# Kernel tuning notes

Measured on AMD Instinct MI355X. Metric: run time of the kernel, lower is better.

The kernel has to match this reference:

```python
import jax, jax.numpy as jnp
import numpy as np

N_NODES = 100000
N_EDGES = 3200000
IN_F, HID_F, OUT_F = 128, 64, 32
NEG_SLOPE = 0.2


def setup_inputs() -> dict:
    key = jax.random.key(0)
    ks = jax.random.split(key, 10)
    glorot = lambda k, shape: jax.random.normal(k, shape, jnp.float32) * jnp.sqrt(2.0 / (shape[0] + shape[-1]))
    x = jax.random.normal(ks[0], (N_NODES, IN_F), jnp.float32)
    edge_index = jax.random.randint(ks[1], (2, N_EDGES), 0, N_NODES, jnp.int64)
    return {
        "x": x,
        "edge_index": edge_index,
        "W1": glorot(ks[2], (IN_F, HID_F)),
        "att_src1": glorot(ks[3], (HID_F,)),
        "att_dst1": glorot(ks[4], (HID_F,)),
        "b1": jnp.zeros((HID_F,), jnp.float32),
        "W2": glorot(ks[5], (HID_F, OUT_F)),
        "att_src2": glorot(ks[6], (OUT_F,)),
        "att_dst2": glorot(ks[7], (OUT_F,)),
        "b2": jnp.zeros((OUT_F,), jnp.float32),
    }


def _segment_softmax(logits, seg, num_segments):
    m = jax.ops.segment_max(logits, seg, num_segments=num_segments)
    e = jnp.exp(logits - m[seg])
    s = jax.ops.segment_sum(e, seg, num_segments=num_segments)
    return e / s[seg]


def _gat_conv(x, src, dst, W, a_src, a_dst, b, n):
    h = x @ W                                    # [N, F]
    logits = jax.nn.leaky_relu((h @ a_src)[src] + (h @ a_dst)[dst], NEG_SLOPE)  # [E]
    att = _segment_softmax(logits, dst, n)       # softmax over incoming edges per dst
    out = jax.ops.segment_sum(h[src] * att[:, None], dst, num_segments=n)
    return out + b


def reference(x, edge_index, W1, att_src1, att_dst1, b1, W2, att_src2, att_dst2, b2):
    n = x.shape[0]
    loops = jnp.arange(n, dtype=edge_index.dtype)
    src = jnp.concatenate([edge_index[0], loops])  # PyG GATConv adds self-loops
    dst = jnp.concatenate([edge_index[1], loops])
    h = _gat_conv(x, src, dst, W1, att_src1, att_dst1, b1, n)
    h = jax.nn.relu(h)
    h = _gat_conv(h, src, dst, W2, att_src2, att_dst2, b2, n)
    return jax.nn.softmax(h, axis=1)
```

## Files before the change

### kernel.cpp

```cpp
#include <hip/hip_runtime.h>

#define N_NODES 100000
#define N_EDGES 3200000
#define ET (N_EDGES + N_NODES)
#define IN_F 128
#define HID_F 64
#define OUT_F 32
#define NEG_SLOPE 0.2f

#define NB 391
#define CHUNK_A 8192
#define BLOCKS_A ((ET + CHUNK_A - 1) / CHUNK_A)
#define BKT_CAP 12288


__global__ __launch_bounds__(256) void histB_kernel(const int* __restrict__ ei,
                                                    int* __restrict__ bcnt) {
    __shared__ int lh[NB];
    for (int i = threadIdx.x; i < NB; i += 256) lh[i] = 0;
    __syncthreads();
    int stride = gridDim.x * 256;
    for (int e = blockIdx.x * 256 + threadIdx.x; e < N_EDGES; e += stride) {
        int dst = ei[N_EDGES + e];
        atomicAdd(&lh[dst >> 8], 1);
    }
    __syncthreads();
    for (int i = threadIdx.x; i < NB; i += 256) {
        int c = lh[i];
        if (c) atomicAdd(&bcnt[i], c);
    }
}


__global__ __launch_bounds__(512) void scanB_kernel(const int* __restrict__ bcnt,
                                                    int* __restrict__ bucket_base,
                                                    int* __restrict__ gcursor,
                                                    int* __restrict__ row_ptr) {
    __shared__ int a[NB];
    int t = threadIdx.x;
    int selfc = 0, cnt = 0;
    if (t < NB) {
        selfc = min(256, N_NODES - (t << 8));
        cnt = bcnt[t] + selfc;
        a[t] = cnt;
    }
    __syncthreads();
    for (int off = 1; off < NB; off <<= 1) {
        int v = 0;
        if (t < NB && t >= off) v = a[t - off];
        __syncthreads();
        if (t < NB) a[t] += v;
        __syncthreads();
    }
    if (t < NB) {
        int base = a[t] - cnt;
        bucket_base[t] = base;
        gcursor[t] = base;
    }
    if (t == 0) { bucket_base[NB] = ET; row_ptr[N_NODES] = ET; }
}


__global__ __launch_bounds__(256) void partA_kernel(const int* __restrict__ ei,
                                                    int* __restrict__ gcursor,
                                                    unsigned* __restrict__ staging) {
    __shared__ int cnt[NB];
    __shared__ int inc[NB];
    __shared__ int delta[NB];
    __shared__ unsigned stg[CHUNK_A];
    __shared__ unsigned short bkt[CHUNK_A];
    int t = threadIdx.x;
    int begin = blockIdx.x * CHUNK_A;
    int n = min(CHUNK_A, ET - begin);

    for (int i = t; i < NB; i += 256) cnt[i] = 0;
    __syncthreads();

    for (int i = t; i < n; i += 256) {
        int e = begin + i;
        int dst = (e < N_EDGES) ? ei[N_EDGES + e] : (e - N_EDGES);
        atomicAdd(&cnt[dst >> 8], 1);
    }
    __syncthreads();

    for (int i = t; i < NB; i += 256) inc[i] = cnt[i];
    __syncthreads();
    for (int off = 1; off < NB; off <<= 1) {
        int i0 = t, i1 = t + 256;
        int v0 = (i0 < NB && i0 >= off) ? inc[i0 - off] : 0;
        int v1 = (i1 < NB && i1 >= off) ? inc[i1 - off] : 0;
        __syncthreads();
        if (i0 < NB) inc[i0] += v0;
        if (i1 < NB) inc[i1] += v1;
        __syncthreads();
    }

    for (int i = t; i < NB; i += 256) {
        int c = cnt[i];
        int ls = inc[i] - c;
        int g = (c > 0) ? atomicAdd(&gcursor[i], c) : 0;
        delta[i] = g - ls;
        cnt[i] = ls;
    }
    __syncthreads();

    for (int i = t; i < n; i += 256) {
        int e = begin + i;
        int src, dst;
        if (e < N_EDGES) { src = ei[e]; dst = ei[N_EDGES + e]; }
        else             { src = dst = e - N_EDGES; }
        int b = dst >> 8;
        int pos = atomicAdd(&cnt[b], 1);
        stg[pos] = ((unsigned)(dst & 255) << 17) | (unsigned)src;
        bkt[pos] = (unsigned short)b;
    }
    __syncthreads();

    for (int i = t; i < n; i += 256) {
        staging[delta[bkt[i]] + i] = stg[i];
    }
}


__global__ __launch_bounds__(256) void partB_kernel(const unsigned* __restrict__ staging,
                                                    const int* __restrict__ bucket_base,
                                                    int* __restrict__ row_ptr,
                                                    int* __restrict__ src_sorted) {
    __shared__ int out_s[BKT_CAP];
    __shared__ int a[256];
    __shared__ int cur[256];
    int b = blockIdx.x, t = threadIdx.x;
    int nb0 = b << 8;
    int nn = min(256, N_NODES - nb0);
    int g0 = bucket_base[b];
    int g1 = bucket_base[b + 1];
    int n = g1 - g0;

    cur[t] = 0;
    __syncthreads();
    for (int i = t; i < n; i += 256)
        atomicAdd(&cur[staging[g0 + i] >> 17], 1);
    __syncthreads();

    int v = cur[t];
    a[t] = v;
    __syncthreads();
    for (int off = 1; off < 256; off <<= 1) {
        int w = (t >= off) ? a[t - off] : 0;
        __syncthreads();
        a[t] += w;
        __syncthreads();
    }
    int pref = a[t] - v;
    cur[t] = pref;
    if (t < nn) row_ptr[nb0 + t] = g0 + pref;
    __syncthreads();

    for (int i = t; i < n; i += 256) {
        unsigned u = staging[g0 + i];
        int pos = atomicAdd(&cur[u >> 17], 1);
        out_s[pos] = (int)(u & 0x1FFFFu);
    }
    __syncthreads();
    for (int i = t; i < n; i += 256)
        src_sorted[g0 + i] = out_s[i];
}


__global__ __launch_bounds__(256) void gemm1_kernel(const float* __restrict__ x,
                                                    const float* __restrict__ W,
                                                    const float* __restrict__ a_src,
                                                    const float* __restrict__ a_dst,
                                                    float* __restrict__ h,
                                                    float* __restrict__ as,
                                                    float* __restrict__ ad) {
    __shared__ float Wl[IN_F * HID_F];
    __shared__ float Xl[64 * 132];
    int t = threadIdx.x;
    int base = blockIdx.x * 64;

    for (int i = t; i < IN_F * HID_F / 4; i += 256)
        ((float4*)Wl)[i] = ((const float4*)W)[i];
#pragma unroll
    for (int i = 0; i < 8; ++i) {
        int f4 = t + 256 * i;
        int r = f4 >> 5, c4 = f4 & 31;
        int gr = base + r; if (gr >= N_NODES) gr = N_NODES - 1;
        ((float4*)Xl)[r * 33 + c4] = ((const float4*)(x + (size_t)gr * IN_F))[c4];
    }
    __syncthreads();

    int tx = t & 15, ty = t >> 4;
    int col = tx * 4, row0 = ty * 4;

    float4 acc0 = {0,0,0,0}, acc1 = {0,0,0,0}, acc2 = {0,0,0,0}, acc3 = {0,0,0,0};

#pragma unroll 4
    for (int k = 0; k < IN_F; k += 4) {
        float4 xv0 = *(const float4*)&Xl[(row0 + 0) * 132 + k];
        float4 xv1 = *(const float4*)&Xl[(row0 + 1) * 132 + k];
        float4 xv2 = *(const float4*)&Xl[(row0 + 2) * 132 + k];
        float4 xv3 = *(const float4*)&Xl[(row0 + 3) * 132 + k];
        float4 wv0 = *(const float4*)&Wl[(k + 0) * HID_F + col];
        float4 wv1 = *(const float4*)&Wl[(k + 1) * HID_F + col];
        float4 wv2 = *(const float4*)&Wl[(k + 2) * HID_F + col];
        float4 wv3 = *(const float4*)&Wl[(k + 3) * HID_F + col];
#define G1STEP(A, XV) \
        A.x = fmaf(XV.x, wv0.x, A.x); A.y = fmaf(XV.x, wv0.y, A.y); \
        A.z = fmaf(XV.x, wv0.z, A.z); A.w = fmaf(XV.x, wv0.w, A.w); \
        A.x = fmaf(XV.y, wv1.x, A.x); A.y = fmaf(XV.y, wv1.y, A.y); \
        A.z = fmaf(XV.y, wv1.z, A.z); A.w = fmaf(XV.y, wv1.w, A.w); \
        A.x = fmaf(XV.z, wv2.x, A.x); A.y = fmaf(XV.z, wv2.y, A.y); \
        A.z = fmaf(XV.z, wv2.z, A.z); A.w = fmaf(XV.z, wv2.w, A.w); \
        A.x = fmaf(XV.w, wv3.x, A.x); A.y = fmaf(XV.w, wv3.y, A.y); \
        A.z = fmaf(XV.w, wv3.z, A.z); A.w = fmaf(XV.w, wv3.w, A.w);
        G1STEP(acc0, xv0) G1STEP(acc1, xv1) G1STEP(acc2, xv2) G1STEP(acc3, xv3)
#undef G1STEP
    }

    float4 av = *(const float4*)&a_src[col];
    float4 dv = *(const float4*)&a_dst[col];
#define G1OUT(I, A) { \
        int grow = base + row0 + I; \
        float vs = A.x*av.x + A.y*av.y + A.z*av.z + A.w*av.w; \
        float vd = A.x*dv.x + A.y*dv.y + A.z*dv.z + A.w*dv.w; \
        vs += __shfl_xor(vs, 1, 64); vd += __shfl_xor(vd, 1, 64); \
        vs += __shfl_xor(vs, 2, 64); vd += __shfl_xor(vd, 2, 64); \
        vs += __shfl_xor(vs, 4, 64); vd += __shfl_xor(vd, 4, 64); \
        vs += __shfl_xor(vs, 8, 64); vd += __shfl_xor(vd, 8, 64); \
        if (grow < N_NODES) { \
            *(float4*)&h[(size_t)grow * HID_F + col] = A; \
            if (tx == 0) { as[grow] = vs; ad[grow] = vd; } \
        } }
    G1OUT(0, acc0) G1OUT(1, acc1) G1OUT(2, acc2) G1OUT(3, acc3)
#undef G1OUT
}


__global__ __launch_bounds__(256) void agg1_kernel(const float* __restrict__ h,
                                                   const float* __restrict__ as,
                                                   const float* __restrict__ ad,
                                                   const int* __restrict__ row_ptr,
                                                   const int* __restrict__ src_sorted,
                                                   const float* __restrict__ b,
                                                   float* __restrict__ r1) {
    int n = blockIdx.x * 4 + (threadIdx.x >> 6);
    int lane = threadIdx.x & 63;
    if (n >= N_NODES) return;
    int beg = row_ptr[n], end = row_ptr[n + 1];
    int deg = end - beg;
    float adn = ad[n];

    int e0 = beg + lane;
    int sidx = 0;
    float l = -1e30f;
    if (e0 < end) {
        sidx = src_sorted[e0];
        float t = as[sidx] + adn;
        l = (t >= 0.f) ? t : NEG_SLOPE * t;
    }
    float m = l;
    float s = (e0 < end) ? 1.f : 0.f;
    for (int e = beg + lane + 64; e < end; e += 64) {
        int s2 = src_sorted[e];
        float t = as[s2] + adn;
        t = (t >= 0.f) ? t : NEG_SLOPE * t;
        float mN = fmaxf(m, t);
        s = s * __expf(m - mN) + __expf(t - mN);
        m = mN;
    }
    for (int off = 32; off > 0; off >>= 1) {
        float mo = __shfl_xor(m, off, 64);
        float so = __shfl_xor(s, off, 64);
        float mN = fmaxf(m, mo);
        s = s * __expf(m - mN) + so * __expf(mo - mN);
        m = mN;
    }
    float inv = 1.f / s;
    float w = __expf(l - m) * inv;

    int g  = lane >> 4;
    int fo = (lane & 15) * 4;
    float4 acc = {0.f, 0.f, 0.f, 0.f};
    int rounds = (min(deg, 64) + 3) >> 2;
    int R4 = (rounds + 3) & ~3;
    for (int k = 0; k < R4; k += 4) {
        float w0 = __shfl(w, (k + 0) * 4 + g, 64);
        float w1 = __shfl(w, (k + 1) * 4 + g, 64);
        float w2 = __shfl(w, (k + 2) * 4 + g, 64);
        float w3 = __shfl(w, (k + 3) * 4 + g, 64);
        int   s0 = __shfl(sidx, (k + 0) * 4 + g, 64);
        int   s1 = __shfl(sidx, (k + 1) * 4 + g, 64);
        int   s2 = __shfl(sidx, (k + 2) * 4 + g, 64);
        int   s3 = __shfl(sidx, (k + 3) * 4 + g, 64);
        float4 p0 = *(const float4*)&h[s0 * HID_F + fo];
        float4 p1 = *(const float4*)&h[s1 * HID_F + fo];
        float4 p2 = *(const float4*)&h[s2 * HID_F + fo];
        float4 p3 = *(const float4*)&h[s3 * HID_F + fo];
        acc.x = fmaf(p0.x, w0, acc.x); acc.y = fmaf(p0.y, w0, acc.y);
        acc.z = fmaf(p0.z, w0, acc.z); acc.w = fmaf(p0.w, w0, acc.w);
        acc.x = fmaf(p1.x, w1, acc.x); acc.y = fmaf(p1.y, w1, acc.y);
        acc.z = fmaf(p1.z, w1, acc.z); acc.w = fmaf(p1.w, w1, acc.w);
        acc.x = fmaf(p2.x, w2, acc.x); acc.y = fmaf(p2.y, w2, acc.y);
        acc.z = fmaf(p2.z, w2, acc.z); acc.w = fmaf(p2.w, w2, acc.w);
        acc.x = fmaf(p3.x, w3, acc.x); acc.y = fmaf(p3.y, w3, acc.y);
        acc.z = fmaf(p3.z, w3, acc.z); acc.w = fmaf(p3.w, w3, acc.w);
    }
    for (int cb = beg + 64; cb < end; cb += 64) {
        int e = cb + lane;
        float wr = 0.f;
        int sr = 0;
        if (e < end) {
            sr = src_sorted[e];
            float t = as[sr] + adn;
            t = (t >= 0.f) ? t : NEG_SLOPE * t;
            wr = __expf(t - m) * inv;
        }
        int cnt = min(64, end - cb);
        int rr = (cnt + 3) >> 2;
        for (int k = 0; k < rr; ++k) {
            int sl = k * 4 + g;
            float wk = __shfl(wr, sl, 64);
            int   sk = __shfl(sr, sl, 64);
            float4 hv = *(const float4*)&h[sk * HID_F + fo];
            acc.x = fmaf(hv.x, wk, acc.x);
            acc.y = fmaf(hv.y, wk, acc.y);
            acc.z = fmaf(hv.z, wk, acc.z);
            acc.w = fmaf(hv.w, wk, acc.w);
        }
    }
    acc.x += __shfl_xor(acc.x, 16, 64); acc.x += __shfl_xor(acc.x, 32, 64);
    acc.y += __shfl_xor(acc.y, 16, 64); acc.y += __shfl_xor(acc.y, 32, 64);
    acc.z += __shfl_xor(acc.z, 16, 64); acc.z += __shfl_xor(acc.z, 32, 64);
    acc.w += __shfl_xor(acc.w, 16, 64); acc.w += __shfl_xor(acc.w, 32, 64);

    if (lane < 16) {
        float4 bv = *(const float4*)&b[fo];
        float4 v;
        v.x = fmaxf(acc.x + bv.x, 0.f);
        v.y = fmaxf(acc.y + bv.y, 0.f);
        v.z = fmaxf(acc.z + bv.z, 0.f);
        v.w = fmaxf(acc.w + bv.w, 0.f);
        *(float4*)&r1[n * HID_F + fo] = v;
    }
}


__global__ __launch_bounds__(256) void gemm2_kernel(const float* __restrict__ r1,
                                                    const float* __restrict__ W,
                                                    const float* __restrict__ a_src,
                                                    const float* __restrict__ a_dst,
                                                    float* __restrict__ h2,
                                                    float* __restrict__ as2,
                                                    float* __restrict__ ad2) {
    __shared__ float Wl[HID_F * OUT_F];
    __shared__ float Xl[128 * 68];
    int t = threadIdx.x;
    int base = blockIdx.x * 128;

    for (int i = t; i < HID_F * OUT_F / 4; i += 256)
        ((float4*)Wl)[i] = ((const float4*)W)[i];
#pragma unroll
    for (int i = 0; i < 8; ++i) {
        int f4 = t + 256 * i;
        int r = f4 >> 4, c4 = f4 & 15;
        int gr = base + r; if (gr >= N_NODES) gr = N_NODES - 1;
        ((float4*)Xl)[r * 17 + c4] = ((const float4*)(r1 + (size_t)gr * HID_F))[c4];
    }
    __syncthreads();

    int tx = t & 7, ty = t >> 3;
    int col = tx * 4, row0 = ty * 4;

    float4 acc0 = {0,0,0,0}, acc1 = {0,0,0,0}, acc2 = {0,0,0,0}, acc3 = {0,0,0,0};

#pragma unroll 4
    for (int k = 0; k < HID_F; k += 4) {
        float4 xv0 = *(const float4*)&Xl[(row0 + 0) * 68 + k];
        float4 xv1 = *(const float4*)&Xl[(row0 + 1) * 68 + k];
        float4 xv2 = *(const float4*)&Xl[(row0 + 2) * 68 + k];
        float4 xv3 = *(const float4*)&Xl[(row0 + 3) * 68 + k];
        float4 wv0 = *(const float4*)&Wl[(k + 0) * OUT_F + col];
        float4 wv1 = *(const float4*)&Wl[(k + 1) * OUT_F + col];
        float4 wv2 = *(const float4*)&Wl[(k + 2) * OUT_F + col];
        float4 wv3 = *(const float4*)&Wl[(k + 3) * OUT_F + col];
#define G2STEP(A, XV) \
        A.x = fmaf(XV.x, wv0.x, A.x); A.y = fmaf(XV.x, wv0.y, A.y); \
        A.z = fmaf(XV.x, wv0.z, A.z); A.w = fmaf(XV.x, wv0.w, A.w); \
        A.x = fmaf(XV.y, wv1.x, A.x); A.y = fmaf(XV.y, wv1.y, A.y); \
        A.z = fmaf(XV.y, wv1.z, A.z); A.w = fmaf(XV.y, wv1.w, A.w); \
        A.x = fmaf(XV.z, wv2.x, A.x); A.y = fmaf(XV.z, wv2.y, A.y); \
        A.z = fmaf(XV.z, wv2.z, A.z); A.w = fmaf(XV.z, wv2.w, A.w); \
        A.x = fmaf(XV.w, wv3.x, A.x); A.y = fmaf(XV.w, wv3.y, A.y); \
        A.z = fmaf(XV.w, wv3.z, A.z); A.w = fmaf(XV.w, wv3.w, A.w);
        G2STEP(acc0, xv0) G2STEP(acc1, xv1) G2STEP(acc2, xv2) G2STEP(acc3, xv3)
#undef G2STEP
    }

    float4 av = *(const float4*)&a_src[col];
    float4 dv = *(const float4*)&a_dst[col];
#define G2OUT(I, A) { \
        int grow = base + row0 + I; \
        float vs = A.x*av.x + A.y*av.y + A.z*av.z + A.w*av.w; \
        float vd = A.x*dv.x + A.y*dv.y + A.z*dv.z + A.w*dv.w; \
        vs += __shfl_xor(vs, 1, 64); vd += __shfl_xor(vd, 1, 64); \
        vs += __shfl_xor(vs, 2, 64); vd += __shfl_xor(vd, 2, 64); \
        vs += __shfl_xor(vs, 4, 64); vd += __shfl_xor(vd, 4, 64); \
        if (grow < N_NODES) { \
            *(float4*)&h2[(size_t)grow * OUT_F + col] = A; \
            if (tx == 0) { as2[grow] = vs; ad2[grow] = vd; } \
        } }
    G2OUT(0, acc0) G2OUT(1, acc1) G2OUT(2, acc2) G2OUT(3, acc3)
#undef G2OUT
}


__global__ __launch_bounds__(256) void agg2_kernel(const float* __restrict__ h2,
                                                   const float* __restrict__ as2,
                                                   const float* __restrict__ ad2,
                                                   const int* __restrict__ row_ptr,
                                                   const int* __restrict__ src_sorted,
                                                   const float* __restrict__ b2,
                                                   float* __restrict__ out) {
    int n = blockIdx.x * 4 + (threadIdx.x >> 6);
    int lane = threadIdx.x & 63;
    if (n >= N_NODES) return;
    int beg = row_ptr[n], end = row_ptr[n + 1];
    int deg = end - beg;
    float adn = ad2[n];

    int e0 = beg + lane;
    int sidx = 0;
    float l = -1e30f;
    if (e0 < end) {
        sidx = src_sorted[e0];
        float t = as2[sidx] + adn;
        l = (t >= 0.f) ? t : NEG_SLOPE * t;
    }
    float m = l;
    float s = (e0 < end) ? 1.f : 0.f;
    for (int e = beg + lane + 64; e < end; e += 64) {
        int s2 = src_sorted[e];
        float t = as2[s2] + adn;
        t = (t >= 0.f) ? t : NEG_SLOPE * t;
        float mN = fmaxf(m, t);
        s = s * __expf(m - mN) + __expf(t - mN);
        m = mN;
    }
    for (int off = 32; off > 0; off >>= 1) {
        float mo = __shfl_xor(m, off, 64);
        float so = __shfl_xor(s, off, 64);
        float mN = fmaxf(m, mo);
        s = s * __expf(m - mN) + so * __expf(mo - mN);
        m = mN;
    }
    float inv = 1.f / s;
    float w = __expf(l - m) * inv;

    int g  = lane >> 3;
    int fo = (lane & 7) * 4;
    float4 acc = {0.f, 0.f, 0.f, 0.f};
    int rounds = (min(deg, 64) + 7) >> 3;
    int R4 = (rounds + 3) & ~3;
    for (int k = 0; k < R4; k += 4) {
        float w0 = __shfl(w, (k + 0) * 8 + g, 64);
        float w1 = __shfl(w, (k + 1) * 8 + g, 64);
        float w2 = __shfl(w, (k + 2) * 8 + g, 64);
        float w3 = __shfl(w, (k + 3) * 8 + g, 64);
        int   s0 = __shfl(sidx, (k + 0) * 8 + g, 64);
        int   s1 = __shfl(sidx, (k + 1) * 8 + g, 64);
        int   s2 = __shfl(sidx, (k + 2) * 8 + g, 64);
        int   s3 = __shfl(sidx, (k + 3) * 8 + g, 64);
        float4 p0 = *(const float4*)&h2[s0 * OUT_F + fo];
        float4 p1 = *(const float4*)&h2[s1 * OUT_F + fo];
        float4 p2 = *(const float4*)&h2[s2 * OUT_F + fo];
        float4 p3 = *(const float4*)&h2[s3 * OUT_F + fo];
        acc.x = fmaf(p0.x, w0, acc.x); acc.y = fmaf(p0.y, w0, acc.y);
        acc.z = fmaf(p0.z, w0, acc.z); acc.w = fmaf(p0.w, w0, acc.w);
        acc.x = fmaf(p1.x, w1, acc.x); acc.y = fmaf(p1.y, w1, acc.y);
        acc.z = fmaf(p1.z, w1, acc.z); acc.w = fmaf(p1.w, w1, acc.w);
        acc.x = fmaf(p2.x, w2, acc.x); acc.y = fmaf(p2.y, w2, acc.y);
        acc.z = fmaf(p2.z, w2, acc.z); acc.w = fmaf(p2.w, w2, acc.w);
        acc.x = fmaf(p3.x, w3, acc.x); acc.y = fmaf(p3.y, w3, acc.y);
        acc.z = fmaf(p3.z, w3, acc.z); acc.w = fmaf(p3.w, w3, acc.w);
    }
    for (int cb = beg + 64; cb < end; cb += 64) {
        int e = cb + lane;
        float wr = 0.f;
        int sr = 0;
        if (e < end) {
            sr = src_sorted[e];
            float t = as2[sr] + adn;
            t = (t >= 0.f) ? t : NEG_SLOPE * t;
            wr = __expf(t - m) * inv;
        }
        int cnt = min(64, end - cb);
        int rr = (cnt + 7) >> 3;
        for (int k = 0; k < rr; ++k) {
            int sl = k * 8 + g;
            float wk = __shfl(wr, sl, 64);
            int   sk = __shfl(sr, sl, 64);
            float4 hv = *(const float4*)&h2[sk * OUT_F + fo];
            acc.x = fmaf(hv.x, wk, acc.x);
            acc.y = fmaf(hv.y, wk, acc.y);
            acc.z = fmaf(hv.z, wk, acc.z);
            acc.w = fmaf(hv.w, wk, acc.w);
        }
    }
    acc.x += __shfl_xor(acc.x, 8, 64); acc.x += __shfl_xor(acc.x, 16, 64); acc.x += __shfl_xor(acc.x, 32, 64);
    acc.y += __shfl_xor(acc.y, 8, 64); acc.y += __shfl_xor(acc.y, 16, 64); acc.y += __shfl_xor(acc.y, 32, 64);
    acc.z += __shfl_xor(acc.z, 8, 64); acc.z += __shfl_xor(acc.z, 16, 64); acc.z += __shfl_xor(acc.z, 32, 64);
    acc.w += __shfl_xor(acc.w, 8, 64); acc.w += __shfl_xor(acc.w, 16, 64); acc.w += __shfl_xor(acc.w, 32, 64);

    float4 bv = *(const float4*)&b2[fo];
    float4 v;
    v.x = acc.x + bv.x; v.y = acc.y + bv.y; v.z = acc.z + bv.z; v.w = acc.w + bv.w;

    float lm = fmaxf(fmaxf(v.x, v.y), fmaxf(v.z, v.w));
    lm = fmaxf(lm, __shfl_xor(lm, 1, 64));
    lm = fmaxf(lm, __shfl_xor(lm, 2, 64));
    lm = fmaxf(lm, __shfl_xor(lm, 4, 64));
    float4 ev;
    ev.x = __expf(v.x - lm); ev.y = __expf(v.y - lm);
    ev.z = __expf(v.z - lm); ev.w = __expf(v.w - lm);
    float ls = ev.x + ev.y + ev.z + ev.w;
    ls += __shfl_xor(ls, 1, 64);
    ls += __shfl_xor(ls, 2, 64);
    ls += __shfl_xor(ls, 4, 64);
    float invs = 1.f / ls;
    if (lane < 8) {
        float4 o;
        o.x = ev.x * invs; o.y = ev.y * invs; o.z = ev.z * invs; o.w = ev.w * invs;
        *(float4*)&out[n * OUT_F + fo] = o;
    }
}


extern "C" void kernel_launch(void* const* d_in, const int* in_sizes, int n_in,
                              void* d_out, int out_size, void* d_ws, size_t ws_size,
                              hipStream_t stream) {
    const float* x     = (const float*)d_in[0];
    const int*   ei    = (const int*)d_in[1];
    const float* W1    = (const float*)d_in[2];
    const float* asrc1 = (const float*)d_in[3];
    const float* adst1 = (const float*)d_in[4];
    const float* b1    = (const float*)d_in[5];
    const float* W2    = (const float*)d_in[6];
    const float* asrc2 = (const float*)d_in[7];
    const float* adst2 = (const float*)d_in[8];
    const float* b2    = (const float*)d_in[9];
    float* out = (float*)d_out;

    char* p = (char*)d_ws;
    auto alloc = [&](size_t bytes) {
        char* q = p;
        p += (bytes + 255) & ~size_t(255);
        return q;
    };
    int*   row_ptr     = (int*)  alloc(sizeof(int) * (N_NODES + 1));
    int*   bcnt        = (int*)  alloc(sizeof(int) * NB);
    int*   bucket_base = (int*)  alloc(sizeof(int) * (NB + 1));
    int*   gcursor     = (int*)  alloc(sizeof(int) * NB);
    int*   src_sorted  = (int*)  alloc(sizeof(int) * (size_t)ET);
    float* h1          = (float*)alloc(sizeof(float) * (size_t)N_NODES * HID_F);
    float* as1         = (float*)alloc(sizeof(float) * N_NODES);
    float* ad1         = (float*)alloc(sizeof(float) * N_NODES);
    float* r1          = (float*)alloc(sizeof(float) * (size_t)N_NODES * HID_F);
    float* h2          = (float*)alloc(sizeof(float) * (size_t)N_NODES * OUT_F);
    float* as2v        = (float*)alloc(sizeof(float) * N_NODES);
    float* ad2v        = (float*)alloc(sizeof(float) * N_NODES);
    unsigned* staging  = (unsigned*)r1;

    hipMemsetAsync(bcnt, 0, sizeof(int) * NB, stream);
    hipLaunchKernelGGL(histB_kernel, dim3(400), dim3(256), 0, stream, ei, bcnt);
    hipLaunchKernelGGL(scanB_kernel, dim3(1), dim3(512), 0, stream,
                       bcnt, bucket_base, gcursor, row_ptr);
    hipLaunchKernelGGL(partA_kernel, dim3(BLOCKS_A), dim3(256), 0, stream, ei, gcursor, staging);
    hipLaunchKernelGGL(partB_kernel, dim3(NB), dim3(256), 0, stream,
                       staging, bucket_base, row_ptr, src_sorted);
    hipLaunchKernelGGL(gemm1_kernel, dim3((N_NODES + 63) / 64), dim3(256), 0, stream,
                       x, W1, asrc1, adst1, h1, as1, ad1);
    hipLaunchKernelGGL(agg1_kernel, dim3((N_NODES + 3) / 4), dim3(256), 0, stream,
                       h1, as1, ad1, row_ptr, src_sorted, b1, r1);
    hipLaunchKernelGGL(gemm2_kernel, dim3((N_NODES + 127) / 128), dim3(256), 0, stream,
                       r1, W2, asrc2, adst2, h2, as2v, ad2v);
    hipLaunchKernelGGL(agg2_kernel, dim3((N_NODES + 3) / 4), dim3(256), 0, stream,
                       h2, as2v, ad2v, row_ptr, src_sorted, b2, out);
}
```

Before: 291.6 us.

## Store layer-1 features in fp16 and batch first-chunk gathers in aggregation

```diff
diff --git a/kernel.cpp b/kernel.cpp
--- a/kernel.cpp
+++ b/kernel.cpp
@@ -1,4 +1,5 @@
 #include <hip/hip_runtime.h>
+#include <hip/hip_fp16.h>
 
 #define N_NODES 100000
 #define N_EDGES 3200000
@@ -171,7 +172,7 @@
                                                     const float* __restrict__ W,
                                                     const float* __restrict__ a_src,
                                                     const float* __restrict__ a_dst,
-                                                    float* __restrict__ h,
+                                                    __half* __restrict__ h,
                                                     float* __restrict__ as,
                                                     float* __restrict__ ad) {
     __shared__ float Wl[IN_F * HID_F];
@@ -229,7 +230,10 @@
         vs += __shfl_xor(vs, 4, 64); vd += __shfl_xor(vd, 4, 64); \
         vs += __shfl_xor(vs, 8, 64); vd += __shfl_xor(vd, 8, 64); \
         if (grow < N_NODES) { \
-            *(float4*)&h[(size_t)grow * HID_F + col] = A; \
+            __half2 p0 = __floats2half2_rn(A.x, A.y); \
+            __half2 p1 = __floats2half2_rn(A.z, A.w); \
+            __half2* hp = (__half2*)&h[(size_t)grow * HID_F + col]; \
+            hp[0] = p0; hp[1] = p1; \
             if (tx == 0) { as[grow] = vs; ad[grow] = vd; } \
         } }
     G1OUT(0, acc0) G1OUT(1, acc1) G1OUT(2, acc2) G1OUT(3, acc3)
@@ -237,7 +241,7 @@
 }
 
 
-__global__ __launch_bounds__(256) void agg1_kernel(const float* __restrict__ h,
+__global__ __launch_bounds__(256) void agg1_kernel(const __half* __restrict__ h,
                                                    const float* __restrict__ as,
                                                    const float* __restrict__ ad,
                                                    const int* __restrict__ row_ptr,
@@ -248,7 +252,6 @@
     int lane = threadIdx.x & 63;
     if (n >= N_NODES) return;
     int beg = row_ptr[n], end = row_ptr[n + 1];
-    int deg = end - beg;
     float adn = ad[n];
 
     int e0 = beg + lane;
@@ -279,33 +282,33 @@
     float inv = 1.f / s;
     float w = __expf(l - m) * inv;
 
-    int g  = lane >> 4;
-    int fo = (lane & 15) * 4;
-    float4 acc = {0.f, 0.f, 0.f, 0.f};
-    int rounds = (min(deg, 64) + 3) >> 2;
-    int R4 = (rounds + 3) & ~3;
-    for (int k = 0; k < R4; k += 4) {
-        float w0 = __shfl(w, (k + 0) * 4 + g, 64);
-        float w1 = __shfl(w, (k + 1) * 4 + g, 64);
-        float w2 = __shfl(w, (k + 2) * 4 + g, 64);
-        float w3 = __shfl(w, (k + 3) * 4 + g, 64);
-        int   s0 = __shfl(sidx, (k + 0) * 4 + g, 64);
-        int   s1 = __shfl(sidx, (k + 1) * 4 + g, 64);
-        int   s2 = __shfl(sidx, (k + 2) * 4 + g, 64);
-        int   s3 = __shfl(sidx, (k + 3) * 4 + g, 64);
-        float4 p0 = *(const float4*)&h[s0 * HID_F + fo];
-        float4 p1 = *(const float4*)&h[s1 * HID_F + fo];
-        float4 p2 = *(const float4*)&h[s2 * HID_F + fo];
-        float4 p3 = *(const float4*)&h[s3 * HID_F + fo];
-        acc.x = fmaf(p0.x, w0, acc.x); acc.y = fmaf(p0.y, w0, acc.y);
-        acc.z = fmaf(p0.z, w0, acc.z); acc.w = fmaf(p0.w, w0, acc.w);
-        acc.x = fmaf(p1.x, w1, acc.x); acc.y = fmaf(p1.y, w1, acc.y);
-        acc.z = fmaf(p1.z, w1, acc.z); acc.w = fmaf(p1.w, w1, acc.w);
-        acc.x = fmaf(p2.x, w2, acc.x); acc.y = fmaf(p2.y, w2, acc.y);
-        acc.z = fmaf(p2.z, w2, acc.z); acc.w = fmaf(p2.w, w2, acc.w);
-        acc.x = fmaf(p3.x, w3, acc.x); acc.y = fmaf(p3.y, w3, acc.y);
-        acc.z = fmaf(p3.z, w3, acc.z); acc.w = fmaf(p3.w, w3, acc.w);
-    }
+    int g  = lane >> 3;
+    int ho = (lane & 7) * 8;
+
+    float ws[8]; int ss[8];
+#pragma unroll
+    for (int k = 0; k < 8; ++k) {
+        ws[k] = __shfl(w,    k * 8 + g, 64);
+        ss[k] = __shfl(sidx, k * 8 + g, 64);
+    }
+    uint4 vv[8];
+#pragma unroll
+    for (int k = 0; k < 8; ++k)
+        vv[k] = *(const uint4*)&h[(size_t)ss[k] * HID_F + ho];
+
+    float4 aL = {0,0,0,0}, aH = {0,0,0,0};
+#define ACC1(V, W) { \
+        float2 f0 = __half22float2(*(const __half2*)&V.x); \
+        float2 f1 = __half22float2(*(const __half2*)&V.y); \
+        float2 f2 = __half22float2(*(const __half2*)&V.z); \
+        float2 f3 = __half22float2(*(const __half2*)&V.w); \
+        aL.x = fmaf(f0.x, W, aL.x); aL.y = fmaf(f0.y, W, aL.y); \
+        aL.z = fmaf(f1.x, W, aL.z); aL.w = fmaf(f1.y, W, aL.w); \
+        aH.x = fmaf(f2.x, W, aH.x); aH.y = fmaf(f2.y, W, aH.y); \
+        aH.z = fmaf(f3.x, W, aH.z); aH.w = fmaf(f3.y, W, aH.w); }
+#pragma unroll
+    for (int k = 0; k < 8; ++k) ACC1(vv[k], ws[k])
+
     for (int cb = beg + 64; cb < end; cb += 64) {
         int e = cb + lane;
         float wr = 0.f;
@@ -317,31 +320,32 @@
             wr = __expf(t - m) * inv;
         }
         int cnt = min(64, end - cb);
-        int rr = (cnt + 3) >> 2;
+        int rr = (cnt + 7) >> 3;
         for (int k = 0; k < rr; ++k) {
-            int sl = k * 4 + g;
-            float wk = __shfl(wr, sl, 64);
-            int   sk = __shfl(sr, sl, 64);
-            float4 hv = *(const float4*)&h[sk * HID_F + fo];
-            acc.x = fmaf(hv.x, wk, acc.x);
-            acc.y = fmaf(hv.y, wk, acc.y);
-            acc.z = fmaf(hv.z, wk, acc.z);
-            acc.w = fmaf(hv.w, wk, acc.w);
+            float wk = __shfl(wr, k * 8 + g, 64);
+            int   sk = __shfl(sr, k * 8 + g, 64);
+            uint4 hv = *(const uint4*)&h[(size_t)sk * HID_F + ho];
+            ACC1(hv, wk)
         }
     }
-    acc.x += __shfl_xor(acc.x, 16, 64); acc.x += __shfl_xor(acc.x, 32, 64);
-    acc.y += __shfl_xor(acc.y, 16, 64); acc.y += __shfl_xor(acc.y, 32, 64);
-    acc.z += __shfl_xor(acc.z, 16, 64); acc.z += __shfl_xor(acc.z, 32, 64);
-    acc.w += __shfl_xor(acc.w, 16, 64); acc.w += __shfl_xor(acc.w, 32, 64);
-
-    if (lane < 16) {
-        float4 bv = *(const float4*)&b[fo];
-        float4 v;
-        v.x = fmaxf(acc.x + bv.x, 0.f);
-        v.y = fmaxf(acc.y + bv.y, 0.f);
-        v.z = fmaxf(acc.z + bv.z, 0.f);
-        v.w = fmaxf(acc.w + bv.w, 0.f);
-        *(float4*)&r1[n * HID_F + fo] = v;
+#undef ACC1
+
+#define RED1(C) C += __shfl_xor(C, 8, 64); C += __shfl_xor(C, 16, 64); C += __shfl_xor(C, 32, 64);
+    RED1(aL.x) RED1(aL.y) RED1(aL.z) RED1(aL.w)
+    RED1(aH.x) RED1(aH.y) RED1(aH.z) RED1(aH.w)
+#undef RED1
+
+    if (lane < 8) {
+        int fo = lane * 8;
+        float4 b0 = *(const float4*)&b[fo];
+        float4 b1 = *(const float4*)&b[fo + 4];
+        float4 vL, vH;
+        vL.x = fmaxf(aL.x + b0.x, 0.f); vL.y = fmaxf(aL.y + b0.y, 0.f);
+        vL.z = fmaxf(aL.z + b0.z, 0.f); vL.w = fmaxf(aL.w + b0.w, 0.f);
+        vH.x = fmaxf(aH.x + b1.x, 0.f); vH.y = fmaxf(aH.y + b1.y, 0.f);
+        vH.z = fmaxf(aH.z + b1.z, 0.f); vH.w = fmaxf(aH.w + b1.w, 0.f);
+        *(float4*)&r1[(size_t)n * HID_F + fo] = vL;
+        *(float4*)&r1[(size_t)n * HID_F + fo + 4] = vH;
     }
 }
 
@@ -426,7 +430,6 @@
     int lane = threadIdx.x & 63;
     if (n >= N_NODES) return;
     int beg = row_ptr[n], end = row_ptr[n + 1];
-    int deg = end - beg;
     float adn = ad2[n];
 
     int e0 = beg + lane;
@@ -459,30 +462,24 @@
 
     int g  = lane >> 3;
     int fo = (lane & 7) * 4;
+    float ws[8]; int ss[8];
+#pragma unroll
+    for (int k = 0; k < 8; ++k) {
+        ws[k] = __shfl(w,    k * 8 + g, 64);
+        ss[k] = __shfl(sidx, k * 8 + g, 64);
+    }
+    float4 p[8];
+#pragma unroll
+    for (int k = 0; k < 8; ++k)
+        p[k] = *(const float4*)&h2[(size_t)ss[k] * OUT_F + fo];
+
     float4 acc = {0.f, 0.f, 0.f, 0.f};
-    int rounds = (min(deg, 64) + 7) >> 3;
-    int R4 = (rounds + 3) & ~3;
-    for (int k = 0; k < R4; k += 4) {
-        float w0 = __shfl(w, (k + 0) * 8 + g, 64);
-        float w1 = __shfl(w, (k + 1) * 8 + g, 64);
-        float w2 = __shfl(w, (k + 2) * 8 + g, 64);
-        float w3 = __shfl(w, (k + 3) * 8 + g, 64);
-        int   s0 = __shfl(sidx, (k + 0) * 8 + g, 64);
-        int   s1 = __shfl(sidx, (k + 1) * 8 + g, 64);
-        int   s2 = __shfl(sidx, (k + 2) * 8 + g, 64);
-        int   s3 = __shfl(sidx, (k + 3) * 8 + g, 64);
-        float4 p0 = *(const float4*)&h2[s0 * OUT_F + fo];
-        float4 p1 = *(const float4*)&h2[s1 * OUT_F + fo];
-        float4 p2 = *(const float4*)&h2[s2 * OUT_F + fo];
-        float4 p3 = *(const float4*)&h2[s3 * OUT_F + fo];
-        acc.x = fmaf(p0.x, w0, acc.x); acc.y = fmaf(p0.y, w0, acc.y);
-        acc.z = fmaf(p0.z, w0, acc.z); acc.w = fmaf(p0.w, w0, acc.w);
-        acc.x = fmaf(p1.x, w1, acc.x); acc.y = fmaf(p1.y, w1, acc.y);
-        acc.z = fmaf(p1.z, w1, acc.z); acc.w = fmaf(p1.w, w1, acc.w);
-        acc.x = fmaf(p2.x, w2, acc.x); acc.y = fmaf(p2.y, w2, acc.y);
-        acc.z = fmaf(p2.z, w2, acc.z); acc.w = fmaf(p2.w, w2, acc.w);
-        acc.x = fmaf(p3.x, w3, acc.x); acc.y = fmaf(p3.y, w3, acc.y);
-        acc.z = fmaf(p3.z, w3, acc.z); acc.w = fmaf(p3.w, w3, acc.w);
+#pragma unroll
+    for (int k = 0; k < 8; ++k) {
+        acc.x = fmaf(p[k].x, ws[k], acc.x);
+        acc.y = fmaf(p[k].y, ws[k], acc.y);
+        acc.z = fmaf(p[k].z, ws[k], acc.z);
+        acc.w = fmaf(p[k].w, ws[k], acc.w);
     }
     for (int cb = beg + 64; cb < end; cb += 64) {
         int e = cb + lane;
@@ -497,10 +494,9 @@
         int cnt = min(64, end - cb);
         int rr = (cnt + 7) >> 3;
         for (int k = 0; k < rr; ++k) {
-            int sl = k * 8 + g;
-            float wk = __shfl(wr, sl, 64);
-            int   sk = __shfl(sr, sl, 64);
-            float4 hv = *(const float4*)&h2[sk * OUT_F + fo];
+            float wk = __shfl(wr, k * 8 + g, 64);
+            int   sk = __shfl(sr, k * 8 + g, 64);
+            float4 hv = *(const float4*)&h2[(size_t)sk * OUT_F + fo];
             acc.x = fmaf(hv.x, wk, acc.x);
             acc.y = fmaf(hv.y, wk, acc.y);
             acc.z = fmaf(hv.z, wk, acc.z);
@@ -531,7 +527,7 @@
     if (lane < 8) {
         float4 o;
         o.x = ev.x * invs; o.y = ev.y * invs; o.z = ev.z * invs; o.w = ev.w * invs;
-        *(float4*)&out[n * OUT_F + fo] = o;
+        *(float4*)&out[(size_t)n * OUT_F + fo] = o;
     }
 }
 
@@ -557,19 +553,19 @@
         p += (bytes + 255) & ~size_t(255);
         return q;
     };
-    int*   row_ptr     = (int*)  alloc(sizeof(int) * (N_NODES + 1));
-    int*   bcnt        = (int*)  alloc(sizeof(int) * NB);
-    int*   bucket_base = (int*)  alloc(sizeof(int) * (NB + 1));
-    int*   gcursor     = (int*)  alloc(sizeof(int) * NB);
-    int*   src_sorted  = (int*)  alloc(sizeof(int) * (size_t)ET);
-    float* h1          = (float*)alloc(sizeof(float) * (size_t)N_NODES * HID_F);
-    float* as1         = (float*)alloc(sizeof(float) * N_NODES);
-    float* ad1         = (float*)alloc(sizeof(float) * N_NODES);
-    float* r1          = (float*)alloc(sizeof(float) * (size_t)N_NODES * HID_F);
-    float* h2          = (float*)alloc(sizeof(float) * (size_t)N_NODES * OUT_F);
-    float* as2v        = (float*)alloc(sizeof(float) * N_NODES);
-    float* ad2v        = (float*)alloc(sizeof(float) * N_NODES);
-    unsigned* staging  = (unsigned*)r1;
+    int*    row_ptr     = (int*)   alloc(sizeof(int) * (N_NODES + 1));
+    int*    bcnt        = (int*)   alloc(sizeof(int) * NB);
+    int*    bucket_base = (int*)   alloc(sizeof(int) * (NB + 1));
+    int*    gcursor     = (int*)   alloc(sizeof(int) * NB);
+    int*    src_sorted  = (int*)   alloc(sizeof(int) * (size_t)ET);
+    __half* h1          = (__half*)alloc(sizeof(__half) * (size_t)N_NODES * HID_F);
+    float*  as1         = (float*) alloc(sizeof(float) * N_NODES);
+    float*  ad1         = (float*) alloc(sizeof(float) * N_NODES);
+    float*  r1          = (float*) alloc(sizeof(float) * (size_t)N_NODES * HID_F);
+    float*  h2          = (float*) alloc(sizeof(float) * (size_t)N_NODES * OUT_F);
+    float*  as2v        = (float*) alloc(sizeof(float) * N_NODES);
+    float*  ad2v        = (float*) alloc(sizeof(float) * N_NODES);
+    unsigned* staging   = (unsigned*)r1;
 
     hipMemsetAsync(bcnt, 0, sizeof(int) * NB, stream);
     hipLaunchKernelGGL(histB_kernel, dim3(400), dim3(256), 0, stream, ei, bcnt);
```

Result: faster. 244.4 us (-16.2%).
